# Optimization experiments

Hardware: AMD Instinct MI355X
Metric: run time of the kernel (lower is better)

## Reference

```python
import jax, jax.numpy as jnp
import numpy as np

EPS = 1e-12  # torch F.normalize eps

def setup_inputs() -> dict:
    key = jax.random.key(0)
    k1, k2, k3, k4 = jax.random.split(key, 4)
    B, S, T, D, r = 8, 50, 77, 1024, 16
    h = jax.random.normal(k1, (B, S, T, D), dtype=jnp.float32)
    # R init: randn / sqrt(D), matching the torch module
    R = jax.random.normal(k2, (S, r, D), dtype=jnp.float32) / np.sqrt(D).astype(np.float32)
    # W, b are zero-init in the module; use small random values so the edit is non-trivial
    W = jax.random.normal(k3, (S, r, D), dtype=jnp.float32) * 0.02
    b = jax.random.normal(k4, (S, r), dtype=jnp.float32) * 0.02
    return {"h": h, "R": R, "W": W, "b": b}

def reference(h, R, W, b):
    # h: (B, S, T, D); R, W: (S, r, D); b: (S, r)
    # Per step t: Phi(h_t) = h_t + Rn_t^T (W_t h_t + b_t - Rn_t h_t), Rn = row-normalized R
    norm = jnp.sqrt(jnp.sum(R * R, axis=-1, keepdims=True))
    Rn = R / jnp.maximum(norm, EPS)
    Rh = jnp.einsum('bstd,srd->bstr', h, Rn)
    Wh = jnp.einsum('bstd,srd->bstr', h, W) + b[None, :, None, :]
    delta = jnp.einsum('bstr,srd->bstd', Wh - Rh, Rn)
    return h + delta
```

## Files before the change

### kernel.cpp

```cpp
#include <hip/hip_runtime.h>


typedef __attribute__((ext_vector_type(8))) short short8;
typedef __attribute__((ext_vector_type(4))) float floatx4;

__device__ __forceinline__ short f2bf(float f) {
  unsigned u = __float_as_uint(f);
  u += 0x7fffu + ((u >> 16) & 1u);
  return (short)(u >> 16);
}

#define S_ 50
#define T_ 77
#define NTOK 616

__global__ __launch_bounds__(256, 2) void loreft_main(
    const float* __restrict__ hG, const float* __restrict__ RG,
    const float* __restrict__ WG, const float* __restrict__ bG,
    float* __restrict__ outG) {
  __shared__ short Ml[16 * 1024];
  __shared__ short Rt[1024 * 16];

  const int s = blockIdx.x;
  const int tid = threadIdx.x;
  const int lane = tid & 63;
  const int wvi = tid >> 6;
  const int m16 = lane & 15;
  const int quad = lane >> 4;

#pragma unroll
  for (int rr = 0; rr < 4; ++rr) {
    const int r = wvi * 4 + rr;
    const floatx4* Rrow = (const floatx4*)(RG + (size_t)((s * 16 + r) << 10));
    const floatx4* Wrow = (const floatx4*)(WG + (size_t)((s * 16 + r) << 10));
    floatx4 rv0 = Rrow[lane * 4 + 0];
    floatx4 rv1 = Rrow[lane * 4 + 1];
    floatx4 rv2 = Rrow[lane * 4 + 2];
    floatx4 rv3 = Rrow[lane * 4 + 3];
    float ss = 0.f;
#pragma unroll
    for (int j = 0; j < 4; ++j)
      ss += rv0[j] * rv0[j] + rv1[j] * rv1[j] + rv2[j] * rv2[j] + rv3[j] * rv3[j];
#pragma unroll
    for (int m = 1; m < 64; m <<= 1) ss += __shfl_xor(ss, m);
    const float inv = 1.0f / fmaxf(sqrtf(ss), 1e-12f);

    floatx4 wa0 = Wrow[lane * 4 + 0];
    floatx4 wa1 = Wrow[lane * 4 + 1];
    floatx4 wa2 = Wrow[lane * 4 + 2];
    floatx4 wa3 = Wrow[lane * 4 + 3];
    float rn[16];
    short8 m0, m1;
#pragma unroll
    for (int j = 0; j < 4; ++j) {
      rn[j]      = rv0[j] * inv;  m0[j]     = f2bf(wa0[j] - rn[j]);
      rn[4 + j]  = rv1[j] * inv;  m0[4 + j] = f2bf(wa1[j] - rn[4 + j]);
      rn[8 + j]  = rv2[j] * inv;  m1[j]     = f2bf(wa2[j] - rn[8 + j]);
      rn[12 + j] = rv3[j] * inv;  m1[4 + j] = f2bf(wa3[j] - rn[12 + j]);
    }
    *(short8*)(Ml + r * 1024 + (((2 * lane) ^ (r & 7)) << 3)) = m0;
    *(short8*)(Ml + r * 1024 + (((2 * lane + 1) ^ (r & 7)) << 3)) = m1;
#pragma unroll
    for (int jj = 0; jj < 16; ++jj)
      Rt[((lane * 16 + jj) << 4) + r] = f2bf(rn[jj]);
  }
  __syncthreads();

  const int tokbase = blockIdx.y * 64 + wvi * 16;
  int tokA = tokbase + m16; if (tokA > NTOK - 1) tokA = NTOK - 1;
  const int bb1 = tokA / T_;
  const int tt1 = tokA - bb1 * T_;
  const size_t rowoff = ((size_t)((bb1 * S_ + s) * T_ + tt1)) << 10;
  const float* hrow = hG + rowoff;
  const floatx4* hrow4 = (const floatx4*)hrow;
  const short* mrow = Ml + m16 * 1024;
  const int msw = m16 & 7;

  floatx4 acc = {0.f, 0.f, 0.f, 0.f};
#pragma unroll 4
  for (int kb = 0; kb < 32; ++kb) {
    floatx4 p0 = hrow4[kb * 8 + quad * 2];
    floatx4 p1 = hrow4[kb * 8 + quad * 2 + 1];
    short8 af;
#pragma unroll
    for (int j = 0; j < 4; ++j) { af[j] = f2bf(p0[j]); af[4 + j] = f2bf(p1[j]); }
    short8 bf = *(const short8*)(mrow + (((kb * 4 + quad) ^ msw) << 3));
    acc = __builtin_amdgcn_mfma_f32_16x16x32_bf16(af, bf, acc, 0, 0, 0);
  }

  const float bias = bG[s * 16 + m16];
  float cf[4];
#pragma unroll
  for (int i = 0; i < 4; ++i) cf[i] = acc[i] + bias;

  unsigned lo = ((unsigned)(unsigned short)f2bf(cf[0])) |
                (((unsigned)(unsigned short)f2bf(cf[1])) << 16);
  unsigned hi = ((unsigned)(unsigned short)f2bf(cf[2])) |
                (((unsigned)(unsigned short)f2bf(cf[3])) << 16);
  short8 bfrag;
  {
    const int srcbase = ((m16 >> 2) << 4) + ((quad & 1) << 3);
    const int regsel = m16 & 3;
#pragma unroll
    for (int j = 0; j < 8; ++j) {
      unsigned vlo = __shfl(lo, srcbase + j);
      unsigned vhi = __shfl(hi, srcbase + j);
      unsigned v32 = (regsel & 2) ? vhi : vlo;
      bfrag[j] = (short)((regsel & 1) ? (v32 >> 16) : (v32 & 0xffffu));
    }
  }
  const short8 zero8 = {0, 0, 0, 0, 0, 0, 0, 0};
  if (quad >= 2) bfrag = zero8;

  float* orow = outG + rowoff;
  const bool valE = (tokbase + m16) < NTOK;
  const int q16 = (quad & 1) << 3;

#pragma unroll 4
  for (int dt = 0; dt < 64; ++dt) {
    short8 t = *(const short8*)(Rt + ((dt * 16 + m16) << 4) + q16);
    short8 ar = (quad < 2) ? t : zero8;
    floatx4 z = {0.f, 0.f, 0.f, 0.f};
    floatx4 dv = __builtin_amdgcn_mfma_f32_16x16x32_bf16(ar, bfrag, z, 0, 0, 0);
    const int d0 = dt * 16 + quad * 4;
    if (valE) {
      floatx4 hv = *(const floatx4*)(hrow + d0);
      floatx4 o;
#pragma unroll
      for (int i = 0; i < 4; ++i) o[i] = hv[i] + dv[i];
      *(floatx4*)(orow + d0) = o;
    }
  }
}

extern "C" void kernel_launch(void* const* d_in, const int* in_sizes, int n_in,
                              void* d_out, int out_size, void* d_ws, size_t ws_size,
                              hipStream_t stream) {
  const float* h = (const float*)d_in[0];
  const float* R = (const float*)d_in[1];
  const float* W = (const float*)d_in[2];
  const float* b = (const float*)d_in[3];
  dim3 grid(S_, 10);
  loreft_main<<<grid, 256, 0, stream>>>(h, R, W, b, (float*)d_out);
}
```

Measured before the change: 263.3 us.

## Split R/W preprocessing into prep kernel and double-buffer loads in main kernel

```diff
diff --git a/kernel.cpp b/kernel.cpp
--- a/kernel.cpp
+++ b/kernel.cpp
@@ -13,6 +13,160 @@
 #define S_ 50
 #define T_ 77
 #define NTOK 616
+
+__global__ __launch_bounds__(256) void prep_kernel(
+    const float* __restrict__ RG, const float* __restrict__ WG,
+    short* __restrict__ Mbf, short* __restrict__ RtT) {
+  const int s = blockIdx.x;
+  const int lane = threadIdx.x & 63;
+  const int wvi = threadIdx.x >> 6;
+#pragma unroll
+  for (int rr = 0; rr < 4; ++rr) {
+    const int r = wvi * 4 + rr;
+    const floatx4* Rrow = (const floatx4*)(RG + ((size_t)(s * 16 + r) << 10));
+    const floatx4* Wrow = (const floatx4*)(WG + ((size_t)(s * 16 + r) << 10));
+    floatx4 rv0 = Rrow[lane * 4 + 0];
+    floatx4 rv1 = Rrow[lane * 4 + 1];
+    floatx4 rv2 = Rrow[lane * 4 + 2];
+    floatx4 rv3 = Rrow[lane * 4 + 3];
+    float ss = 0.f;
+#pragma unroll
+    for (int j = 0; j < 4; ++j)
+      ss += rv0[j] * rv0[j] + rv1[j] * rv1[j] + rv2[j] * rv2[j] + rv3[j] * rv3[j];
+#pragma unroll
+    for (int m = 1; m < 64; m <<= 1) ss += __shfl_xor(ss, m);
+    const float inv = 1.0f / fmaxf(sqrtf(ss), 1e-12f);
+
+    floatx4 wa0 = Wrow[lane * 4 + 0];
+    floatx4 wa1 = Wrow[lane * 4 + 1];
+    floatx4 wa2 = Wrow[lane * 4 + 2];
+    floatx4 wa3 = Wrow[lane * 4 + 3];
+    float rn[16];
+    short8 m0, m1;
+#pragma unroll
+    for (int j = 0; j < 4; ++j) {
+      rn[j]      = rv0[j] * inv;  m0[j]     = f2bf(wa0[j] - rn[j]);
+      rn[4 + j]  = rv1[j] * inv;  m0[4 + j] = f2bf(wa1[j] - rn[4 + j]);
+      rn[8 + j]  = rv2[j] * inv;  m1[j]     = f2bf(wa2[j] - rn[8 + j]);
+      rn[12 + j] = rv3[j] * inv;  m1[4 + j] = f2bf(wa3[j] - rn[12 + j]);
+    }
+    short* mrow = Mbf + ((size_t)(s * 16 + r) << 10);
+    *(short8*)(mrow + lane * 16) = m0;
+    *(short8*)(mrow + lane * 16 + 8) = m1;
+    short* rt = RtT + ((size_t)s << 14);
+#pragma unroll
+    for (int jj = 0; jj < 16; ++jj)
+      rt[((lane * 16 + jj) << 4) + r] = f2bf(rn[jj]);
+  }
+}
+
+__global__ __launch_bounds__(256, 2) void loreft_fast(
+    const float* __restrict__ hG, const float* __restrict__ bG,
+    const short* __restrict__ Mbf, const short* __restrict__ RtT,
+    float* __restrict__ outG) {
+  const int s = blockIdx.x;
+  const int lane = threadIdx.x & 63;
+  const int wvi = threadIdx.x >> 6;
+  const int m16 = lane & 15;
+  const int quad = lane >> 4;
+
+  const int tokbase = blockIdx.y * 64 + wvi * 16;
+  int tokA = tokbase + m16; if (tokA > NTOK - 1) tokA = NTOK - 1;
+  const int bb = tokA / T_;
+  const int tt = tokA - bb * T_;
+  const size_t rowoff = ((size_t)((bb * S_ + s) * T_ + tt)) << 10;
+  const floatx4* hrow4 = (const floatx4*)(hG + rowoff);
+  const short* mrow = Mbf + ((size_t)(s * 16 + m16) << 10);
+
+  floatx4 hbuf[2][8];
+  short8 mbuf[2][4];
+#pragma unroll
+  for (int u = 0; u < 4; ++u) {
+    hbuf[0][2 * u]     = hrow4[u * 8 + quad * 2];
+    hbuf[0][2 * u + 1] = hrow4[u * 8 + quad * 2 + 1];
+    mbuf[0][u]         = *(const short8*)(mrow + u * 32 + quad * 8);
+  }
+  floatx4 acc = {0.f, 0.f, 0.f, 0.f};
+#pragma unroll
+  for (int ch = 0; ch < 8; ++ch) {
+    const int cur = ch & 1, nxt = cur ^ 1;
+    if (ch < 7) {
+#pragma unroll
+      for (int u = 0; u < 4; ++u) {
+        const int kb = (ch + 1) * 4 + u;
+        hbuf[nxt][2 * u]     = hrow4[kb * 8 + quad * 2];
+        hbuf[nxt][2 * u + 1] = hrow4[kb * 8 + quad * 2 + 1];
+        mbuf[nxt][u]         = *(const short8*)(mrow + kb * 32 + quad * 8);
+      }
+    }
+#pragma unroll
+    for (int u = 0; u < 4; ++u) {
+      short8 af;
+#pragma unroll
+      for (int j = 0; j < 4; ++j) {
+        af[j]     = f2bf(hbuf[cur][2 * u][j]);
+        af[4 + j] = f2bf(hbuf[cur][2 * u + 1][j]);
+      }
+      acc = __builtin_amdgcn_mfma_f32_16x16x32_bf16(af, mbuf[cur][u], acc, 0, 0, 0);
+    }
+  }
+
+  const float bias = bG[s * 16 + m16];
+  float cf[4];
+#pragma unroll
+  for (int i = 0; i < 4; ++i) cf[i] = acc[i] + bias;
+
+  unsigned lo = ((unsigned)(unsigned short)f2bf(cf[0])) |
+                (((unsigned)(unsigned short)f2bf(cf[1])) << 16);
+  unsigned hi = ((unsigned)(unsigned short)f2bf(cf[2])) |
+                (((unsigned)(unsigned short)f2bf(cf[3])) << 16);
+  short8 bfrag;
+  {
+    const int srcbase = ((m16 >> 2) << 4) + ((quad & 1) << 3);
+    const int regsel = m16 & 3;
+#pragma unroll
+    for (int j = 0; j < 8; ++j) {
+      unsigned vlo = __shfl(lo, srcbase + j);
+      unsigned vhi = __shfl(hi, srcbase + j);
+      unsigned v32 = (regsel & 2) ? vhi : vlo;
+      bfrag[j] = (short)((regsel & 1) ? (v32 >> 16) : (v32 & 0xffffu));
+    }
+  }
+  const short8 zero8 = {0, 0, 0, 0, 0, 0, 0, 0};
+  if (quad >= 2) bfrag = zero8;
+
+  const short* rt = RtT + ((size_t)s << 14);
+  floatx4* orow4 = (floatx4*)(outG + rowoff);
+  const bool valE = (tokbase + m16) < NTOK;
+  const int q8 = (quad & 1) << 3;
+
+  short8 rtb[2][4];
+  floatx4 hb2[2][4];
+#pragma unroll
+  for (int u = 0; u < 4; ++u) {
+    rtb[0][u] = *(const short8*)(rt + ((u * 16 + m16) << 4) + q8);
+    hb2[0][u] = hrow4[u * 4 + quad];
+  }
+#pragma unroll
+  for (int ch = 0; ch < 16; ++ch) {
+    const int cur = ch & 1, nxt = cur ^ 1;
+    if (ch < 15) {
+#pragma unroll
+      for (int u = 0; u < 4; ++u) {
+        const int dt = (ch + 1) * 4 + u;
+        rtb[nxt][u] = *(const short8*)(rt + ((dt * 16 + m16) << 4) + q8);
+        hb2[nxt][u] = hrow4[dt * 4 + quad];
+      }
+    }
+#pragma unroll
+    for (int u = 0; u < 4; ++u) {
+      const int dt = ch * 4 + u;
+      short8 ar = (quad < 2) ? rtb[cur][u] : zero8;
+      floatx4 o = __builtin_amdgcn_mfma_f32_16x16x32_bf16(ar, bfrag, hb2[cur][u], 0, 0, 0);
+      if (valE) orow4[dt * 4 + quad] = o;
+    }
+  }
+}
 
 __global__ __launch_bounds__(256, 2) void loreft_main(
     const float* __restrict__ hG, const float* __restrict__ RG,
@@ -140,6 +294,14 @@
   const float* R = (const float*)d_in[1];
   const float* W = (const float*)d_in[2];
   const float* b = (const float*)d_in[3];
+  const size_t need = (size_t)2 * 50 * 16 * 1024 * sizeof(short);
   dim3 grid(S_, 10);
-  loreft_main<<<grid, 256, 0, stream>>>(h, R, W, b, (float*)d_out);
-}
+  if (ws_size >= need) {
+    short* Mbf = (short*)d_ws;
+    short* RtT = Mbf + (size_t)50 * 16 * 1024;
+    prep_kernel<<<50, 256, 0, stream>>>(R, W, Mbf, RtT);
+    loreft_fast<<<grid, 256, 0, stream>>>(h, b, Mbf, RtT, (float*)d_out);
+  } else {
+    loreft_main<<<grid, 256, 0, stream>>>(h, R, W, b, (float*)d_out);
+  }
+}
```

After: 276.4 us. 1.05x slower.

## Split weight prep into separate kernel and split-K tokens across waves

Applied to the files above, without the earlier changes.

```diff
diff --git a/kernel.cpp b/kernel.cpp
--- a/kernel.cpp
+++ b/kernel.cpp
@@ -14,12 +14,55 @@
 #define T_ 77
 #define NTOK 616
 
-__global__ __launch_bounds__(256, 2) void loreft_main(
-    const float* __restrict__ hG, const float* __restrict__ RG,
-    const float* __restrict__ WG, const float* __restrict__ bG,
+__global__ __launch_bounds__(256) void prep_kernel(
+    const float* __restrict__ RG, const float* __restrict__ WG,
+    short* __restrict__ Mbf, short* __restrict__ RtT) {
+  const int wid = blockIdx.x * 4 + (threadIdx.x >> 6);
+  const int lane = threadIdx.x & 63;
+  const int s = wid >> 4, r = wid & 15;
+
+  const floatx4* Rrow = (const floatx4*)(RG + ((size_t)wid << 10));
+  const floatx4* Wrow = (const floatx4*)(WG + ((size_t)wid << 10));
+  floatx4 rv0 = Rrow[lane * 4 + 0];
+  floatx4 rv1 = Rrow[lane * 4 + 1];
+  floatx4 rv2 = Rrow[lane * 4 + 2];
+  floatx4 rv3 = Rrow[lane * 4 + 3];
+  float ss = 0.f;
+#pragma unroll
+  for (int j = 0; j < 4; ++j)
+    ss += rv0[j] * rv0[j] + rv1[j] * rv1[j] + rv2[j] * rv2[j] + rv3[j] * rv3[j];
+#pragma unroll
+  for (int m = 1; m < 64; m <<= 1) ss += __shfl_xor(ss, m);
+  const float inv = 1.0f / fmaxf(sqrtf(ss), 1e-12f);
+
+  floatx4 wa0 = Wrow[lane * 4 + 0];
+  floatx4 wa1 = Wrow[lane * 4 + 1];
+  floatx4 wa2 = Wrow[lane * 4 + 2];
+  floatx4 wa3 = Wrow[lane * 4 + 3];
+  float rn[16];
+  short8 m0, m1;
+#pragma unroll
+  for (int j = 0; j < 4; ++j) {
+    rn[j]      = rv0[j] * inv;  m0[j]     = f2bf(wa0[j] - rn[j]);
+    rn[4 + j]  = rv1[j] * inv;  m0[4 + j] = f2bf(wa1[j] - rn[4 + j]);
+    rn[8 + j]  = rv2[j] * inv;  m1[j]     = f2bf(wa2[j] - rn[8 + j]);
+    rn[12 + j] = rv3[j] * inv;  m1[4 + j] = f2bf(wa3[j] - rn[12 + j]);
+  }
+  short* mrow = Mbf + ((size_t)wid << 10);
+  *(short8*)(mrow + lane * 16) = m0;
+  *(short8*)(mrow + lane * 16 + 8) = m1;
+  short* rt = RtT + ((size_t)s << 14);
+#pragma unroll
+  for (int jj = 0; jj < 16; ++jj)
+    rt[((lane * 16 + jj) << 4) + r] = f2bf(rn[jj]);
+}
+
+__global__ __launch_bounds__(256, 4) void loreft_fast(
+    const float* __restrict__ hG, const float* __restrict__ bG,
+    const short* __restrict__ Mbf, const short* __restrict__ RtT,
     float* __restrict__ outG) {
-  __shared__ short Ml[16 * 1024];
-  __shared__ short Rt[1024 * 16];
+  __shared__ float redbuf[4 * 256];
+  __shared__ short cbuf[256];
 
   const int s = blockIdx.x;
   const int tid = threadIdx.x;
@@ -28,108 +71,60 @@
   const int m16 = lane & 15;
   const int quad = lane >> 4;
 
+  const int tokbase = blockIdx.y * 16;
+  int tokA = tokbase + m16; if (tokA > NTOK - 1) tokA = NTOK - 1;
+  const int bb = tokA / T_;
+  const int tt = tokA - bb * T_;
+  const size_t rowoff = ((size_t)((bb * S_ + s) * T_ + tt)) << 10;
+  const floatx4* hrow4 = (const floatx4*)(hG + rowoff);
+
+  const int wofs = wvi * 256;
+  const short* mrow = Mbf + ((size_t)(s * 16 + m16) << 10) + wofs;
+  const floatx4* hk = hrow4 + (wofs >> 2);
+
+  floatx4 acc = {0.f, 0.f, 0.f, 0.f};
 #pragma unroll
-  for (int rr = 0; rr < 4; ++rr) {
-    const int r = wvi * 4 + rr;
-    const floatx4* Rrow = (const floatx4*)(RG + (size_t)((s * 16 + r) << 10));
-    const floatx4* Wrow = (const floatx4*)(WG + (size_t)((s * 16 + r) << 10));
-    floatx4 rv0 = Rrow[lane * 4 + 0];
-    floatx4 rv1 = Rrow[lane * 4 + 1];
-    floatx4 rv2 = Rrow[lane * 4 + 2];
-    floatx4 rv3 = Rrow[lane * 4 + 3];
-    float ss = 0.f;
+  for (int kb = 0; kb < 8; ++kb) {
+    floatx4 p0 = hk[kb * 8 + quad * 2];
+    floatx4 p1 = hk[kb * 8 + quad * 2 + 1];
+    short8 bfr = *(const short8*)(mrow + kb * 32 + quad * 8);
+    short8 af;
 #pragma unroll
-    for (int j = 0; j < 4; ++j)
-      ss += rv0[j] * rv0[j] + rv1[j] * rv1[j] + rv2[j] * rv2[j] + rv3[j] * rv3[j];
+    for (int j = 0; j < 4; ++j) { af[j] = f2bf(p0[j]); af[4 + j] = f2bf(p1[j]); }
+    acc = __builtin_amdgcn_mfma_f32_16x16x32_bf16(af, bfr, acc, 0, 0, 0);
+  }
+  {
+    float* rb = redbuf + wvi * 256;
 #pragma unroll
-    for (int m = 1; m < 64; m <<= 1) ss += __shfl_xor(ss, m);
-    const float inv = 1.0f / fmaxf(sqrtf(ss), 1e-12f);
-
-    floatx4 wa0 = Wrow[lane * 4 + 0];
-    floatx4 wa1 = Wrow[lane * 4 + 1];
-    floatx4 wa2 = Wrow[lane * 4 + 2];
-    floatx4 wa3 = Wrow[lane * 4 + 3];
-    float rn[16];
-    short8 m0, m1;
-#pragma unroll
-    for (int j = 0; j < 4; ++j) {
-      rn[j]      = rv0[j] * inv;  m0[j]     = f2bf(wa0[j] - rn[j]);
-      rn[4 + j]  = rv1[j] * inv;  m0[4 + j] = f2bf(wa1[j] - rn[4 + j]);
-      rn[8 + j]  = rv2[j] * inv;  m1[j]     = f2bf(wa2[j] - rn[8 + j]);
-      rn[12 + j] = rv3[j] * inv;  m1[4 + j] = f2bf(wa3[j] - rn[12 + j]);
-    }
-    *(short8*)(Ml + r * 1024 + (((2 * lane) ^ (r & 7)) << 3)) = m0;
-    *(short8*)(Ml + r * 1024 + (((2 * lane + 1) ^ (r & 7)) << 3)) = m1;
-#pragma unroll
-    for (int jj = 0; jj < 16; ++jj)
-      Rt[((lane * 16 + jj) << 4) + r] = f2bf(rn[jj]);
+    for (int i = 0; i < 4; ++i)
+      rb[(quad * 4 + i) * 16 + m16] = acc[i];
+  }
+  __syncthreads();
+  {
+    const int tok = tid >> 4, r = tid & 15;
+    const int o = tok * 16 + r;
+    float c = redbuf[o] + redbuf[256 + o] + redbuf[512 + o] + redbuf[768 + o]
+            + bG[s * 16 + r];
+    cbuf[o] = f2bf(c);
   }
   __syncthreads();
 
-  const int tokbase = blockIdx.y * 64 + wvi * 16;
-  int tokA = tokbase + m16; if (tokA > NTOK - 1) tokA = NTOK - 1;
-  const int bb1 = tokA / T_;
-  const int tt1 = tokA - bb1 * T_;
-  const size_t rowoff = ((size_t)((bb1 * S_ + s) * T_ + tt1)) << 10;
-  const float* hrow = hG + rowoff;
-  const floatx4* hrow4 = (const floatx4*)hrow;
-  const short* mrow = Ml + m16 * 1024;
-  const int msw = m16 & 7;
+  const short8 zero8 = {0, 0, 0, 0, 0, 0, 0, 0};
+  short8 bfrag = (quad < 2) ? *(const short8*)(cbuf + m16 * 16 + quad * 8)
+                            : zero8;
 
-  floatx4 acc = {0.f, 0.f, 0.f, 0.f};
-#pragma unroll 4
-  for (int kb = 0; kb < 32; ++kb) {
-    floatx4 p0 = hrow4[kb * 8 + quad * 2];
-    floatx4 p1 = hrow4[kb * 8 + quad * 2 + 1];
-    short8 af;
+  const short* rt = RtT + ((size_t)s << 14);
+  floatx4* orow4 = (floatx4*)(outG + rowoff);
+  const bool valE = (tokbase + m16) < NTOK;
+  const int q8 = (quad & 1) << 3;
+
 #pragma unroll
-    for (int j = 0; j < 4; ++j) { af[j] = f2bf(p0[j]); af[4 + j] = f2bf(p1[j]); }
-    short8 bf = *(const short8*)(mrow + (((kb * 4 + quad) ^ msw) << 3));
-    acc = __builtin_amdgcn_mfma_f32_16x16x32_bf16(af, bf, acc, 0, 0, 0);
-  }
-
-  const float bias = bG[s * 16 + m16];
-  float cf[4];
-#pragma unroll
-  for (int i = 0; i < 4; ++i) cf[i] = acc[i] + bias;
-
-  unsigned lo = ((unsigned)(unsigned short)f2bf(cf[0])) |
-                (((unsigned)(unsigned short)f2bf(cf[1])) << 16);
-  unsigned hi = ((unsigned)(unsigned short)f2bf(cf[2])) |
-                (((unsigned)(unsigned short)f2bf(cf[3])) << 16);
-  short8 bfrag;
-  {
-    const int srcbase = ((m16 >> 2) << 4) + ((quad & 1) << 3);
-    const int regsel = m16 & 3;
-#pragma unroll
-    for (int j = 0; j < 8; ++j) {
-      unsigned vlo = __shfl(lo, srcbase + j);
-      unsigned vhi = __shfl(hi, srcbase + j);
-      unsigned v32 = (regsel & 2) ? vhi : vlo;
-      bfrag[j] = (short)((regsel & 1) ? (v32 >> 16) : (v32 & 0xffffu));
-    }
-  }
-  const short8 zero8 = {0, 0, 0, 0, 0, 0, 0, 0};
-  if (quad >= 2) bfrag = zero8;
-
-  float* orow = outG + rowoff;
-  const bool valE = (tokbase + m16) < NTOK;
-  const int q16 = (quad & 1) << 3;
-
-#pragma unroll 4
-  for (int dt = 0; dt < 64; ++dt) {
-    short8 t = *(const short8*)(Rt + ((dt * 16 + m16) << 4) + q16);
-    short8 ar = (quad < 2) ? t : zero8;
-    floatx4 z = {0.f, 0.f, 0.f, 0.f};
-    floatx4 dv = __builtin_amdgcn_mfma_f32_16x16x32_bf16(ar, bfrag, z, 0, 0, 0);
-    const int d0 = dt * 16 + quad * 4;
-    if (valE) {
-      floatx4 hv = *(const floatx4*)(hrow + d0);
-      floatx4 o;
-#pragma unroll
-      for (int i = 0; i < 4; ++i) o[i] = hv[i] + dv[i];
-      *(floatx4*)(orow + d0) = o;
-    }
+  for (int u = 0; u < 16; ++u) {
+    const int dt = wvi * 16 + u;
+    short8 ar = *(const short8*)(rt + ((dt * 16 + m16) << 4) + q8);
+    floatx4 hv = hrow4[dt * 4 + quad];
+    floatx4 o = __builtin_amdgcn_mfma_f32_16x16x32_bf16(ar, bfrag, hv, 0, 0, 0);
+    if (valE) orow4[dt * 4 + quad] = o;
   }
 }
 
@@ -140,6 +135,9 @@
   const float* R = (const float*)d_in[1];
   const float* W = (const float*)d_in[2];
   const float* b = (const float*)d_in[3];
-  dim3 grid(S_, 10);
-  loreft_main<<<grid, 256, 0, stream>>>(h, R, W, b, (float*)d_out);
+  short* Mbf = (short*)d_ws;
+  short* RtT = Mbf + (size_t)50 * 16 * 1024;
+  prep_kernel<<<200, 256, 0, stream>>>(R, W, Mbf, RtT);
+  dim3 grid(S_, 39);
+  loreft_fast<<<grid, 256, 0, stream>>>(h, b, Mbf, RtT, (float*)d_out);
 }
```

Result: slower. 291.8 us (+10.8%).
